# Kernel optimization log

Hardware: AMD Instinct MI355X
Metric: run time of the kernel (lower is better)

## Reference

```python
import jax, jax.numpy as jnp
import numpy as np

B, S, D, H = 2, 2048, 1024, 16
DH = D // H  # 64
NEG = -1000000000.0


def setup_inputs() -> dict:
    key = jax.random.key(0)
    ks = jax.random.split(key, 10)
    scale = 1.0 / np.sqrt(D)
    inp = {
        "x": jax.random.normal(ks[0], (B, S, D), dtype=jnp.float32),
        "mask": jax.random.randint(ks[1], (B, S, S), 0, 2, dtype=jnp.int32),
        "Wq": jax.random.normal(ks[2], (D, D), dtype=jnp.float32) * scale,
        "bq": jnp.zeros((D,), dtype=jnp.float32),
        "Wk": jax.random.normal(ks[3], (D, D), dtype=jnp.float32) * scale,
        "bk": jnp.zeros((D,), dtype=jnp.float32),
        "Wv": jax.random.normal(ks[4], (D, D), dtype=jnp.float32) * scale,
        "bv": jnp.zeros((D,), dtype=jnp.float32),
        "Wo": jax.random.normal(ks[5], (D, D), dtype=jnp.float32) * scale,
        "bo": jnp.zeros((D,), dtype=jnp.float32),
    }
    return inp


def reference(x, mask, Wq, bq, Wk, bk, Wv, bv, Wo, bo):
    b, s, _ = x.shape
    # Linear projections (torch Linear: y = x @ W^T + b), then split heads -> [b,h,s,dh]
    q = (x @ Wq.T + bq).reshape(b, s, H, DH).transpose(0, 2, 1, 3)
    k = (x @ Wk.T + bk).reshape(b, s, H, DH).transpose(0, 2, 1, 3)
    v = (x @ Wv.T + bv).reshape(b, s, H, DH).transpose(0, 2, 1, 3)
    # scores: [b,h,sq,sk]
    scores = jnp.einsum("bhqd,bhkd->bhqk", q, k) / jnp.sqrt(jnp.float32(DH))
    # code masks where mask == 0 (mask broadcast over heads)
    scores = jnp.where(mask[:, None, :, :] == 0, NEG, scores)
    attn = jax.nn.softmax(scores, axis=-1)
    out = jnp.einsum("bhqk,bhkd->bhqd", attn, v)  # [b,h,sq,dh]
    out = out.transpose(0, 2, 1, 3).reshape(b, s, D)  # merge heads -> [b,s,d]
    return out @ Wo.T + bo
```

## Files before the change

### kernel.cpp

```cpp
#include <hip/hip_runtime.h>
#include <stdint.h>

#define SB 2
#define SS 2048
#define SD 1024
#define SH 16
#define SDH 64
#define SM (SB*SS)
#define NEGINF_MASK -1000000000.0f
#define QSCALE 0.18033688011112043f
#define CSHIFT 16.0f

typedef __attribute__((ext_vector_type(8))) short short8;
typedef __attribute__((ext_vector_type(4))) short short4v;
typedef __attribute__((ext_vector_type(4))) float f32x4;
typedef __attribute__((ext_vector_type(4))) float float4v;
typedef __attribute__((ext_vector_type(2))) uint32_t uint2v;

__device__ static inline short f2bf(float f) {
    uint32_t u = __float_as_uint(f);
    u += 0x7fffu + ((u >> 16) & 1u);
    return (short)(u >> 16);
}

__device__ static inline void gload_lds16(const void* g, void* l) {
    __builtin_amdgcn_global_load_lds(
        (__attribute__((address_space(1))) void*)g,
        (__attribute__((address_space(3))) void*)l,
        16, 0, 0);
}

#define NX4 (SM*SD/4)
#define NW4 (SD*SD/4)
__global__ void cvt_all_kernel(const float* __restrict__ x,
                               const float* __restrict__ Wq, const float* __restrict__ Wk,
                               const float* __restrict__ Wv, const float* __restrict__ Wo,
                               short* __restrict__ xb,
                               short* __restrict__ wqb, short* __restrict__ wkb,
                               short* __restrict__ wvb, short* __restrict__ wob) {
    int i = blockIdx.x * 256 + threadIdx.x;
    const float* src; short* dst; int idx;
    if (i < NX4) { src = x; dst = xb; idx = i; }
    else {
        int j = i - NX4;
        int sel = j >> 18;
        idx = j & (NW4 - 1);
        src = (sel == 0) ? Wq : (sel == 1) ? Wk : (sel == 2) ? Wv : Wo;
        dst = (sel == 0) ? wqb : (sel == 1) ? wkb : (sel == 2) ? wvb : wob;
    }
    float4v v = *(const float4v*)(src + (size_t)idx * 4);
    short4v o;
    o[0] = f2bf(v[0]); o[1] = f2bf(v[1]); o[2] = f2bf(v[2]); o[3] = f2bf(v[3]);
    *(short4v*)(dst + (size_t)idx * 4) = o;
}

__global__ void pack_mask_kernel(const int* __restrict__ mask, unsigned long long* __restrict__ bits) {
    unsigned int i = blockIdx.x * 256u + threadIdx.x;
    int pred = mask[i] != 0;
    unsigned long long b = __ballot(pred);
    if ((threadIdx.x & 63u) == 0u) bits[i >> 6] = b;
}

template <typename OutT>
__device__ inline void gemm_bt_body(const short* __restrict__ A, const short* __restrict__ W,
                                    const float* __restrict__ bias, OutT* __restrict__ C,
                                    int M, int N, int K, int rowBase, int colBase, float scale) {
    __shared__ short As[2][128 * 32];
    __shared__ short Bs[2][128 * 32];
    const int tid = threadIdx.x, lane = tid & 63, wid = tid >> 6;
    const int r15 = lane & 15, hi = lane >> 4;
    const int wr = wid >> 1, wc = wid & 1;

    const int chBase0 = wid * 64, chBase1 = 256 + wid * 64;
    const int ch0 = chBase0 + lane, ch1 = chBase1 + lane;
    const short* aP0 = A + (size_t)(rowBase + (ch0 >> 2)) * K + (ch0 & 3) * 8;
    const short* aP1 = A + (size_t)(rowBase + (ch1 >> 2)) * K + (ch1 & 3) * 8;
    const short* bP0 = W + (size_t)(colBase + (ch0 >> 2)) * K + (ch0 & 3) * 8;
    const short* bP1 = W + (size_t)(colBase + (ch1 >> 2)) * K + (ch1 & 3) * 8;

    gload_lds16(aP0, &As[0][chBase0 * 8]);
    gload_lds16(aP1, &As[0][chBase1 * 8]);
    gload_lds16(bP0, &Bs[0][chBase0 * 8]);
    gload_lds16(bP1, &Bs[0][chBase1 * 8]);

    f32x4 acc[4][4] = {};
    const int NIT = K / 32;

    for (int it = 0; it < NIT; ++it) {
        __syncthreads();
        const int cur = it & 1, nxt = cur ^ 1;
        if (it + 1 < NIT) {
            int kt = (it + 1) * 32;
            gload_lds16(aP0 + kt, &As[nxt][chBase0 * 8]);
            gload_lds16(aP1 + kt, &As[nxt][chBase1 * 8]);
            gload_lds16(bP0 + kt, &Bs[nxt][chBase0 * 8]);
            gload_lds16(bP1 + kt, &Bs[nxt][chBase1 * 8]);
        }

        short8 aF[4], bF[4];
#pragma unroll
        for (int mi = 0; mi < 4; ++mi)
            aF[mi] = *(const short8*)&As[cur][(wr * 64 + mi * 16 + r15) * 32 + hi * 8];
#pragma unroll
        for (int ni = 0; ni < 4; ++ni)
            bF[ni] = *(const short8*)&Bs[cur][(wc * 64 + ni * 16 + r15) * 32 + hi * 8];

        __builtin_amdgcn_s_setprio(1);
#pragma unroll
        for (int mi = 0; mi < 4; ++mi)
#pragma unroll
            for (int ni = 0; ni < 4; ++ni)
                acc[mi][ni] = __builtin_amdgcn_mfma_f32_16x16x32_bf16(aF[mi], bF[ni], acc[mi][ni], 0, 0, 0);
        __builtin_amdgcn_s_setprio(0);
    }

#pragma unroll
    for (int ni = 0; ni < 4; ++ni) {
        int col = colBase + wc * 64 + ni * 16 + r15;
        float bv = bias[col];
#pragma unroll
        for (int mi = 0; mi < 4; ++mi) {
#pragma unroll
            for (int r = 0; r < 4; ++r) {
                int row = rowBase + wr * 64 + mi * 16 + hi * 4 + r;
                float v = (acc[mi][ni][r] + bv) * scale;
                if constexpr (sizeof(OutT) == 2) C[(size_t)row * N + col] = f2bf(v);
                else                             C[(size_t)row * N + col] = v;
            }
        }
    }
}

__global__ __launch_bounds__(256, 3) void gemm_qkv_kernel(
    const short* __restrict__ A,
    const short* __restrict__ W0, const short* __restrict__ W1, const short* __restrict__ W2,
    const float* __restrict__ b0, const float* __restrict__ b1, const float* __restrict__ b2,
    short* __restrict__ O0, short* __restrict__ O1, short* __restrict__ O2) {
    const short* W = (blockIdx.z == 0) ? W0 : (blockIdx.z == 1) ? W1 : W2;
    const float* bias = (blockIdx.z == 0) ? b0 : (blockIdx.z == 1) ? b1 : b2;
    short* C = (blockIdx.z == 0) ? O0 : (blockIdx.z == 1) ? O1 : O2;
    float scale = (blockIdx.z == 0) ? QSCALE : 1.0f;
    gemm_bt_body<short>(A, W, bias, C, SM, SD, SD, blockIdx.y * 128, blockIdx.x * 128, scale);
}

__global__ __launch_bounds__(256, 3) void gemm_out_kernel(
    const short* __restrict__ A, const short* __restrict__ W,
    const float* __restrict__ bias, float* __restrict__ C) {
    gemm_bt_body<float>(A, W, bias, C, SM, SD, SD, blockIdx.y * 128, blockIdx.x * 128, 1.0f);
}

__global__ __launch_bounds__(512, 4) void attn_kernel(
    const short* __restrict__ Q, const short* __restrict__ K, const short* __restrict__ V,
    const unsigned long long* __restrict__ mbits, short* __restrict__ O) {
    const int tid = threadIdx.x, lane = tid & 63, wid = tid >> 6;
    const int r15 = lane & 15, hi = lane >> 4;
    const int b = blockIdx.z, h = blockIdx.y;
    const int q0 = blockIdx.x * 128 + wid * 16;
    const int brow = b * SS;

    __shared__ short Ks[2][64 * 64];
    __shared__ short Vt[2][64 * 72];
    __shared__ short Pl[8][16 * 64];
    char* pw = (char*)&Pl[wid][0];

    const short* Kbase = K + (size_t)brow * SD + h * SDH;
    const short* Vbase = V + (size_t)brow * SD + h * SDH;
    const unsigned long long* mrow_p = mbits + (size_t)(brow + q0 + r15) * (SS / 64);

    short8 qF[2];
#pragma unroll
    for (int kd = 0; kd < 2; ++kd)
        qF[kd] = *(const short8*)&Q[(size_t)(brow + q0 + r15) * SD + h * SDH + kd * 32 + hi * 8];

    short8 onesF;
#pragma unroll
    for (int j = 0; j < 8; ++j) onesF[j] = (short)0x3F80;

    f32x4 o[4] = {};
    f32x4 lacc = {};

    const int krow_s = tid >> 3, kcol_s = tid & 7;
    const int vp = tid & 31, vc0 = (tid >> 5) * 4;

    gload_lds16(Kbase + (size_t)krow_s * SD + ((kcol_s ^ (krow_s & 7)) * 8), &Ks[0][wid * 512]);
    short4v va = *(const short4v*)(Vbase + (size_t)(2 * vp) * SD + vc0);
    short4v vb2 = *(const short4v*)(Vbase + (size_t)(2 * vp + 1) * SD + vc0);
    unsigned long long mb = mrow_p[0];
#pragma unroll
    for (int j = 0; j < 4; ++j) {
        uint32_t pk = (uint32_t)(uint16_t)va[j] | ((uint32_t)(uint16_t)vb2[j] << 16);
        *(uint32_t*)&Vt[0][(vc0 + j) * 72 + 2 * vp] = pk;
    }

    for (int t = 0; t < SS / 64; ++t) {
        __syncthreads();
        const int cur = t & 1, nxt = cur ^ 1;
        const int tn = (t < SS / 64 - 1) ? t + 1 : t;

        gload_lds16(Kbase + (size_t)(tn * 64 + krow_s) * SD + ((kcol_s ^ (krow_s & 7)) * 8),
                    &Ks[nxt][wid * 512]);
        va  = *(const short4v*)(Vbase + (size_t)(tn * 64 + 2 * vp) * SD + vc0);
        vb2 = *(const short4v*)(Vbase + (size_t)(tn * 64 + 2 * vp + 1) * SD + vc0);
        unsigned long long mbn = mrow_p[tn];

        f32x4 s[4] = {};
        __builtin_amdgcn_s_setprio(1);
#pragma unroll
        for (int kc = 0; kc < 4; ++kc) {
            int krow = kc * 16 + r15;
#pragma unroll
            for (int kd = 0; kd < 2; ++kd) {
                short8 kF = *(const short8*)&Ks[cur][krow * 64 + (((kd * 4 + hi) ^ (krow & 7)) * 8)];
                s[kc] = __builtin_amdgcn_mfma_f32_16x16x32_bf16(kF, qF[kd], s[kc], 0, 0, 0);
            }
        }
        __builtin_amdgcn_s_setprio(0);

#pragma unroll
        for (int kc = 0; kc < 4; ++kc) {
            unsigned nib = (unsigned)(mb >> (kc * 16 + hi * 4)) & 0xFu;
#pragma unroll
            for (int r = 0; r < 4; ++r) {
                float v = (nib & (1u << r)) ? (s[kc][r] - CSHIFT) : NEGINF_MASK;
                float e;
                asm("v_exp_f32 %0, %1" : "=v"(e) : "v"(v));
                s[kc][r] = e;
            }
        }

#pragma unroll
        for (int kc = 0; kc < 4; ++kc) {
            uint32_t d0, d1;
            asm("v_cvt_pk_bf16_f32 %0, %1, %2" : "=v"(d0) : "v"(s[kc][0]), "v"(s[kc][1]));
            asm("v_cvt_pk_bf16_f32 %0, %1, %2" : "=v"(d1) : "v"(s[kc][2]), "v"(s[kc][3]));
            int chunk = (2 * kc + (hi >> 1)) ^ (r15 & 7);
            uint2v val = { d0, d1 };
            *(uint2v*)(pw + r15 * 128 + chunk * 16 + (hi & 1) * 8) = val;
        }

        short8 pF[2];
#pragma unroll
        for (int kf = 0; kf < 2; ++kf) {
            int chunk = (4 * kf + hi) ^ (r15 & 7);
            pF[kf] = *(const short8*)(pw + r15 * 128 + chunk * 16);
        }

        __builtin_amdgcn_s_setprio(1);
#pragma unroll
        for (int df = 0; df < 4; ++df) {
#pragma unroll
            for (int kf = 0; kf < 2; ++kf) {
                short8 vF = *(const short8*)&Vt[cur][(df * 16 + r15) * 72 + kf * 32 + hi * 8];
                o[df] = __builtin_amdgcn_mfma_f32_16x16x32_bf16(pF[kf], vF, o[df], 0, 0, 0);
            }
        }
        lacc = __builtin_amdgcn_mfma_f32_16x16x32_bf16(pF[0], onesF, lacc, 0, 0, 0);
        lacc = __builtin_amdgcn_mfma_f32_16x16x32_bf16(pF[1], onesF, lacc, 0, 0, 0);
        __builtin_amdgcn_s_setprio(0);

#pragma unroll
        for (int j = 0; j < 4; ++j) {
            uint32_t pk = (uint32_t)(uint16_t)va[j] | ((uint32_t)(uint16_t)vb2[j] << 16);
            *(uint32_t*)&Vt[nxt][(vc0 + j) * 72 + 2 * vp] = pk;
        }
        mb = mbn;
    }

#pragma unroll
    for (int r = 0; r < 4; ++r) {
        float inv = 1.0f / lacc[r];
        size_t row = (size_t)(brow + q0 + hi * 4 + r);
#pragma unroll
        for (int df = 0; df < 4; ++df)
            O[row * SD + h * SDH + df * 16 + r15] = f2bf(o[df][r] * inv);
    }
}

extern "C" void kernel_launch(void* const* d_in, const int* in_sizes, int n_in,
                              void* d_out, int out_size, void* d_ws, size_t ws_size,
                              hipStream_t stream) {
    const float* x  = (const float*)d_in[0];
    const int* mask = (const int*)d_in[1];
    const float* Wq = (const float*)d_in[2];
    const float* bq = (const float*)d_in[3];
    const float* Wk = (const float*)d_in[4];
    const float* bk = (const float*)d_in[5];
    const float* Wv = (const float*)d_in[6];
    const float* bv = (const float*)d_in[7];
    const float* Wo = (const float*)d_in[8];
    const float* bo = (const float*)d_in[9];
    float* out = (float*)d_out;

    char* ws = (char*)d_ws;
    size_t off = 0;
    auto alloc = [&](size_t bytes) { void* p = ws + off; off += (bytes + 255) & ~(size_t)255; return p; };

    short* xb  = (short*)alloc((size_t)SM * SD * 2);
    short* wqb = (short*)alloc((size_t)SD * SD * 2);
    short* wkb = (short*)alloc((size_t)SD * SD * 2);
    short* wvb = (short*)alloc((size_t)SD * SD * 2);
    short* wob = (short*)alloc((size_t)SD * SD * 2);
    short* Qb  = (short*)alloc((size_t)SM * SD * 2);
    short* Kb  = (short*)alloc((size_t)SM * SD * 2);
    short* Vb  = (short*)alloc((size_t)SM * SD * 2);
    short* AOb = (short*)alloc((size_t)SM * SD * 2);
    unsigned long long* mbits = (unsigned long long*)alloc((size_t)SB * SS * (SS / 64) * 8);

    cvt_all_kernel<<<(NX4 + 4 * NW4) / 256, 256, 0, stream>>>(
        x, Wq, Wk, Wv, Wo, xb, wqb, wkb, wvb, wob);
    pack_mask_kernel<<<SB * SS * SS / 256, 256, 0, stream>>>(mask, mbits);

    gemm_qkv_kernel<<<dim3(SD / 128, SM / 128, 3), 256, 0, stream>>>(
        xb, wqb, wkb, wvb, bq, bk, bv, Qb, Kb, Vb);

    attn_kernel<<<dim3(SS / 128, SH, SB), 512, 0, stream>>>(Qb, Kb, Vb, mbits, AOb);

    gemm_out_kernel<<<dim3(SD / 128, SM / 128), 256, 0, stream>>>(AOb, wob, bo, out);
}
```

Measured before the change: 148.7 us.

## Split attention waves into 2x4 query/key-half grid with LDS partial-sum reduction

```diff
diff --git a/kernel.cpp b/kernel.cpp
--- a/kernel.cpp
+++ b/kernel.cpp
@@ -155,7 +155,8 @@
     const int tid = threadIdx.x, lane = tid & 63, wid = tid >> 6;
     const int r15 = lane & 15, hi = lane >> 4;
     const int b = blockIdx.z, h = blockIdx.y;
-    const int q0 = blockIdx.x * 128 + wid * 16;
+    const int qc = wid & 3, kh = wid >> 2;
+    const int q0 = blockIdx.x * 128 + qc * 32;
     const int brow = b * SS;
 
     __shared__ short Ks[2][64 * 64];
@@ -165,19 +166,22 @@
 
     const short* Kbase = K + (size_t)brow * SD + h * SDH;
     const short* Vbase = V + (size_t)brow * SD + h * SDH;
-    const unsigned long long* mrow_p = mbits + (size_t)(brow + q0 + r15) * (SS / 64);
-
-    short8 qF[2];
-#pragma unroll
-    for (int kd = 0; kd < 2; ++kd)
-        qF[kd] = *(const short8*)&Q[(size_t)(brow + q0 + r15) * SD + h * SDH + kd * 32 + hi * 8];
+    const unsigned long long* mp0 = mbits + (size_t)(brow + q0 + r15) * (SS / 64);
+    const unsigned long long* mp1 = mbits + (size_t)(brow + q0 + 16 + r15) * (SS / 64);
+
+    short8 qF[2][2];
+#pragma unroll
+    for (int c = 0; c < 2; ++c)
+#pragma unroll
+        for (int kd = 0; kd < 2; ++kd)
+            qF[c][kd] = *(const short8*)&Q[(size_t)(brow + q0 + c * 16 + r15) * SD + h * SDH + kd * 32 + hi * 8];
 
     short8 onesF;
 #pragma unroll
     for (int j = 0; j < 8; ++j) onesF[j] = (short)0x3F80;
 
-    f32x4 o[4] = {};
-    f32x4 lacc = {};
+    f32x4 o[2][4] = {};
+    f32x4 lacc[2] = {};
 
     const int krow_s = tid >> 3, kcol_s = tid & 7;
     const int vp = tid & 31, vc0 = (tid >> 5) * 4;
@@ -185,7 +189,7 @@
     gload_lds16(Kbase + (size_t)krow_s * SD + ((kcol_s ^ (krow_s & 7)) * 8), &Ks[0][wid * 512]);
     short4v va = *(const short4v*)(Vbase + (size_t)(2 * vp) * SD + vc0);
     short4v vb2 = *(const short4v*)(Vbase + (size_t)(2 * vp + 1) * SD + vc0);
-    unsigned long long mb = mrow_p[0];
+    unsigned long long mb[2] = { mp0[0], mp1[0] };
 #pragma unroll
     for (int j = 0; j < 4; ++j) {
         uint32_t pk = (uint32_t)(uint16_t)va[j] | ((uint32_t)(uint16_t)vb2[j] << 16);
@@ -201,61 +205,57 @@
                     &Ks[nxt][wid * 512]);
         va  = *(const short4v*)(Vbase + (size_t)(tn * 64 + 2 * vp) * SD + vc0);
         vb2 = *(const short4v*)(Vbase + (size_t)(tn * 64 + 2 * vp + 1) * SD + vc0);
-        unsigned long long mbn = mrow_p[tn];
-
-        f32x4 s[4] = {};
+        unsigned long long mbn0 = mp0[tn], mbn1 = mp1[tn];
+
+        f32x4 s[2][2] = {};
         __builtin_amdgcn_s_setprio(1);
 #pragma unroll
-        for (int kc = 0; kc < 4; ++kc) {
-            int krow = kc * 16 + r15;
+        for (int kc = 0; kc < 2; ++kc) {
+            int krow = kh * 32 + kc * 16 + r15;
 #pragma unroll
             for (int kd = 0; kd < 2; ++kd) {
                 short8 kF = *(const short8*)&Ks[cur][krow * 64 + (((kd * 4 + hi) ^ (krow & 7)) * 8)];
-                s[kc] = __builtin_amdgcn_mfma_f32_16x16x32_bf16(kF, qF[kd], s[kc], 0, 0, 0);
+                s[0][kc] = __builtin_amdgcn_mfma_f32_16x16x32_bf16(kF, qF[0][kd], s[0][kc], 0, 0, 0);
+                s[1][kc] = __builtin_amdgcn_mfma_f32_16x16x32_bf16(kF, qF[1][kd], s[1][kc], 0, 0, 0);
             }
         }
         __builtin_amdgcn_s_setprio(0);
 
-#pragma unroll
-        for (int kc = 0; kc < 4; ++kc) {
-            unsigned nib = (unsigned)(mb >> (kc * 16 + hi * 4)) & 0xFu;
-#pragma unroll
-            for (int r = 0; r < 4; ++r) {
-                float v = (nib & (1u << r)) ? (s[kc][r] - CSHIFT) : NEGINF_MASK;
-                float e;
-                asm("v_exp_f32 %0, %1" : "=v"(e) : "v"(v));
-                s[kc][r] = e;
+        short8 pF[2];
+#pragma unroll
+        for (int c = 0; c < 2; ++c) {
+            unsigned long long mbc = (c == 0) ? mb[0] : mb[1];
+            char* pc = pw + c * 1024;
+#pragma unroll
+            for (int kc = 0; kc < 2; ++kc) {
+                unsigned nib = (unsigned)(mbc >> (kh * 32 + kc * 16 + hi * 4)) & 0xFu;
+#pragma unroll
+                for (int r = 0; r < 4; ++r) {
+                    float v = (nib & (1u << r)) ? (s[c][kc][r] - CSHIFT) : NEGINF_MASK;
+                    float e;
+                    asm("v_exp_f32 %0, %1" : "=v"(e) : "v"(v));
+                    s[c][kc][r] = e;
+                }
+                uint32_t d0, d1;
+                asm("v_cvt_pk_bf16_f32 %0, %1, %2" : "=v"(d0) : "v"(s[c][kc][0]), "v"(s[c][kc][1]));
+                asm("v_cvt_pk_bf16_f32 %0, %1, %2" : "=v"(d1) : "v"(s[c][kc][2]), "v"(s[c][kc][3]));
+                int chunk = (2 * kc + (hi >> 1)) ^ (r15 & 3);
+                uint2v val = { d0, d1 };
+                *(uint2v*)(pc + r15 * 64 + chunk * 16 + (hi & 1) * 8) = val;
             }
-        }
-
-#pragma unroll
-        for (int kc = 0; kc < 4; ++kc) {
-            uint32_t d0, d1;
-            asm("v_cvt_pk_bf16_f32 %0, %1, %2" : "=v"(d0) : "v"(s[kc][0]), "v"(s[kc][1]));
-            asm("v_cvt_pk_bf16_f32 %0, %1, %2" : "=v"(d1) : "v"(s[kc][2]), "v"(s[kc][3]));
-            int chunk = (2 * kc + (hi >> 1)) ^ (r15 & 7);
-            uint2v val = { d0, d1 };
-            *(uint2v*)(pw + r15 * 128 + chunk * 16 + (hi & 1) * 8) = val;
-        }
-
-        short8 pF[2];
-#pragma unroll
-        for (int kf = 0; kf < 2; ++kf) {
-            int chunk = (4 * kf + hi) ^ (r15 & 7);
-            pF[kf] = *(const short8*)(pw + r15 * 128 + chunk * 16);
+            int rchunk = hi ^ (r15 & 3);
+            pF[c] = *(const short8*)(pc + r15 * 64 + rchunk * 16);
         }
 
         __builtin_amdgcn_s_setprio(1);
 #pragma unroll
         for (int df = 0; df < 4; ++df) {
-#pragma unroll
-            for (int kf = 0; kf < 2; ++kf) {
-                short8 vF = *(const short8*)&Vt[cur][(df * 16 + r15) * 72 + kf * 32 + hi * 8];
-                o[df] = __builtin_amdgcn_mfma_f32_16x16x32_bf16(pF[kf], vF, o[df], 0, 0, 0);
-            }
-        }
-        lacc = __builtin_amdgcn_mfma_f32_16x16x32_bf16(pF[0], onesF, lacc, 0, 0, 0);
-        lacc = __builtin_amdgcn_mfma_f32_16x16x32_bf16(pF[1], onesF, lacc, 0, 0, 0);
+            short8 vF = *(const short8*)&Vt[cur][(df * 16 + r15) * 72 + kh * 32 + hi * 8];
+            o[0][df] = __builtin_amdgcn_mfma_f32_16x16x32_bf16(pF[0], vF, o[0][df], 0, 0, 0);
+            o[1][df] = __builtin_amdgcn_mfma_f32_16x16x32_bf16(pF[1], vF, o[1][df], 0, 0, 0);
+        }
+        lacc[0] = __builtin_amdgcn_mfma_f32_16x16x32_bf16(pF[0], onesF, lacc[0], 0, 0, 0);
+        lacc[1] = __builtin_amdgcn_mfma_f32_16x16x32_bf16(pF[1], onesF, lacc[1], 0, 0, 0);
         __builtin_amdgcn_s_setprio(0);
 
 #pragma unroll
@@ -263,17 +263,59 @@
             uint32_t pk = (uint32_t)(uint16_t)va[j] | ((uint32_t)(uint16_t)vb2[j] << 16);
             *(uint32_t*)&Vt[nxt][(vc0 + j) * 72 + 2 * vp] = pk;
         }
-        mb = mbn;
-    }
-
-#pragma unroll
-    for (int r = 0; r < 4; ++r) {
-        float inv = 1.0f / lacc[r];
-        size_t row = (size_t)(brow + q0 + hi * 4 + r);
-#pragma unroll
-        for (int df = 0; df < 4; ++df)
-            O[row * SD + h * SDH + df * 16 + r15] = f2bf(o[df][r] * inv);
-    }
+        mb[0] = mbn0; mb[1] = mbn1;
+    }
+
+    float* lbase = (float*)&Ks[0][0];
+    float* obase = (float*)&Pl[0][0];
+
+#define PUBLISH(slot)                                                            \
+    {                                                                            \
+        float* mbf = obase + (slot) * 2048;                                      \
+        _Pragma("unroll")                                                        \
+        for (int c = 0; c < 2; ++c)                                              \
+            _Pragma("unroll")                                                    \
+            for (int df = 0; df < 4; ++df)                                       \
+                _Pragma("unroll")                                                \
+                for (int r = 0; r < 4; ++r)                                      \
+                    mbf[(c * 16 + hi * 4 + r) * 64 + df * 16 + r15] = o[c][df][r]; \
+        if (r15 == 0) {                                                          \
+            _Pragma("unroll")                                                    \
+            for (int c = 0; c < 2; ++c)                                          \
+                _Pragma("unroll")                                                \
+                for (int r = 0; r < 4; ++r)                                      \
+                    lbase[(slot) * 32 + c * 16 + hi * 4 + r] = lacc[c][r];       \
+        }                                                                        \
+    }
+
+#define CONSUME(slot)                                                            \
+    {                                                                            \
+        float* mbf = obase + (slot) * 2048;                                      \
+        _Pragma("unroll")                                                        \
+        for (int c = 0; c < 2; ++c)                                              \
+            _Pragma("unroll")                                                    \
+            for (int r = 0; r < 4; ++r) {                                        \
+                float lt = lacc[c][r] + lbase[(slot) * 32 + c * 16 + hi * 4 + r];\
+                float inv = 1.0f / lt;                                           \
+                size_t row = (size_t)(brow + q0 + c * 16 + hi * 4 + r);          \
+                _Pragma("unroll")                                                \
+                for (int df = 0; df < 4; ++df) {                                 \
+                    float ot = o[c][df][r] + mbf[(c * 16 + hi * 4 + r) * 64 + df * 16 + r15]; \
+                    O[row * SD + h * SDH + df * 16 + r15] = f2bf(ot * inv);      \
+                }                                                                \
+            }                                                                    \
+    }
+
+    __syncthreads();
+    if (kh == 1 && qc < 2) PUBLISH(qc);
+    __syncthreads();
+    if (kh == 0 && qc < 2) CONSUME(qc);
+    __syncthreads();
+    if (kh == 1 && qc >= 2) PUBLISH(qc - 2);
+    __syncthreads();
+    if (kh == 0 && qc >= 2) CONSUME(qc - 2);
+#undef PUBLISH
+#undef CONSUME
 }
 
 extern "C" void kernel_launch(void* const* d_in, const int* in_sizes, int n_in,
```

Result: slower. 154.4 us (+3.9%).

## Keep softmax probabilities in registers via permuted V layout; retile output GEMM

Applied to the files above, without the earlier changes.

```diff
diff --git a/kernel.cpp b/kernel.cpp
--- a/kernel.cpp
+++ b/kernel.cpp
@@ -15,7 +15,7 @@
 typedef __attribute__((ext_vector_type(4))) short short4v;
 typedef __attribute__((ext_vector_type(4))) float f32x4;
 typedef __attribute__((ext_vector_type(4))) float float4v;
-typedef __attribute__((ext_vector_type(2))) uint32_t uint2v;
+typedef __attribute__((ext_vector_type(4))) uint32_t uint4v;
 
 __device__ static inline short f2bf(float f) {
     uint32_t u = __float_as_uint(f);
@@ -61,10 +61,18 @@
     if ((threadIdx.x & 63u) == 0u) bits[i >> 6] = b;
 }
 
-template <typename OutT>
-__device__ inline void gemm_bt_body(const short* __restrict__ A, const short* __restrict__ W,
-                                    const float* __restrict__ bias, OutT* __restrict__ C,
-                                    int M, int N, int K, int rowBase, int colBase, float scale) {
+__global__ __launch_bounds__(256, 3) void gemm_qkv_kernel(
+    const short* __restrict__ A,
+    const short* __restrict__ W0, const short* __restrict__ W1, const short* __restrict__ W2,
+    const float* __restrict__ b0, const float* __restrict__ b1, const float* __restrict__ b2,
+    short* __restrict__ O0, short* __restrict__ O1, short* __restrict__ O2) {
+    const short* W = (blockIdx.z == 0) ? W0 : (blockIdx.z == 1) ? W1 : W2;
+    const float* bias = (blockIdx.z == 0) ? b0 : (blockIdx.z == 1) ? b1 : b2;
+    short* C = (blockIdx.z == 0) ? O0 : (blockIdx.z == 1) ? O1 : O2;
+    const float scale = (blockIdx.z == 0) ? QSCALE : 1.0f;
+    const int rowBase = blockIdx.y * 128, colBase = blockIdx.x * 128;
+    const int K = SD, N = SD;
+
     __shared__ short As[2][128 * 32];
     __shared__ short Bs[2][128 * 32];
     const int tid = threadIdx.x, lane = tid & 63, wid = tid >> 6;
@@ -123,30 +131,76 @@
 #pragma unroll
             for (int r = 0; r < 4; ++r) {
                 int row = rowBase + wr * 64 + mi * 16 + hi * 4 + r;
-                float v = (acc[mi][ni][r] + bv) * scale;
-                if constexpr (sizeof(OutT) == 2) C[(size_t)row * N + col] = f2bf(v);
-                else                             C[(size_t)row * N + col] = v;
-            }
-        }
-    }
-}
-
-__global__ __launch_bounds__(256, 3) void gemm_qkv_kernel(
-    const short* __restrict__ A,
-    const short* __restrict__ W0, const short* __restrict__ W1, const short* __restrict__ W2,
-    const float* __restrict__ b0, const float* __restrict__ b1, const float* __restrict__ b2,
-    short* __restrict__ O0, short* __restrict__ O1, short* __restrict__ O2) {
-    const short* W = (blockIdx.z == 0) ? W0 : (blockIdx.z == 1) ? W1 : W2;
-    const float* bias = (blockIdx.z == 0) ? b0 : (blockIdx.z == 1) ? b1 : b2;
-    short* C = (blockIdx.z == 0) ? O0 : (blockIdx.z == 1) ? O1 : O2;
-    float scale = (blockIdx.z == 0) ? QSCALE : 1.0f;
-    gemm_bt_body<short>(A, W, bias, C, SM, SD, SD, blockIdx.y * 128, blockIdx.x * 128, scale);
-}
-
-__global__ __launch_bounds__(256, 3) void gemm_out_kernel(
+                C[(size_t)row * N + col] = f2bf((acc[mi][ni][r] + bv) * scale);
+            }
+        }
+    }
+}
+
+__global__ __launch_bounds__(256, 2) void gemm_out_kernel(
     const short* __restrict__ A, const short* __restrict__ W,
     const float* __restrict__ bias, float* __restrict__ C) {
-    gemm_bt_body<float>(A, W, bias, C, SM, SD, SD, blockIdx.y * 128, blockIdx.x * 128, 1.0f);
+    const int rowBase = blockIdx.y * 128, colBase = blockIdx.x * 64;
+    const int K = SD, N = SD;
+
+    __shared__ short As[2][128 * 32];
+    __shared__ short Bs[2][64 * 32];
+    const int tid = threadIdx.x, lane = tid & 63, wid = tid >> 6;
+    const int r15 = lane & 15, hi = lane >> 4;
+
+    const int chBase0 = wid * 64, chBase1 = 256 + wid * 64;
+    const int ch0 = chBase0 + lane, ch1 = chBase1 + lane;
+    const short* aP0 = A + (size_t)(rowBase + (ch0 >> 2)) * K + (ch0 & 3) * 8;
+    const short* aP1 = A + (size_t)(rowBase + (ch1 >> 2)) * K + (ch1 & 3) * 8;
+    const short* bP0 = W + (size_t)(colBase + (ch0 >> 2)) * K + (ch0 & 3) * 8;
+
+    gload_lds16(aP0, &As[0][chBase0 * 8]);
+    gload_lds16(aP1, &As[0][chBase1 * 8]);
+    gload_lds16(bP0, &Bs[0][chBase0 * 8]);
+
+    f32x4 acc[2][4] = {};
+    const int NIT = K / 32;
+
+    for (int it = 0; it < NIT; ++it) {
+        __syncthreads();
+        const int cur = it & 1, nxt = cur ^ 1;
+        if (it + 1 < NIT) {
+            int kt = (it + 1) * 32;
+            gload_lds16(aP0 + kt, &As[nxt][chBase0 * 8]);
+            gload_lds16(aP1 + kt, &As[nxt][chBase1 * 8]);
+            gload_lds16(bP0 + kt, &Bs[nxt][chBase0 * 8]);
+        }
+
+        short8 aF[2], bF[4];
+#pragma unroll
+        for (int mi = 0; mi < 2; ++mi)
+            aF[mi] = *(const short8*)&As[cur][(wid * 32 + mi * 16 + r15) * 32 + hi * 8];
+#pragma unroll
+        for (int ni = 0; ni < 4; ++ni)
+            bF[ni] = *(const short8*)&Bs[cur][(ni * 16 + r15) * 32 + hi * 8];
+
+        __builtin_amdgcn_s_setprio(1);
+#pragma unroll
+        for (int mi = 0; mi < 2; ++mi)
+#pragma unroll
+            for (int ni = 0; ni < 4; ++ni)
+                acc[mi][ni] = __builtin_amdgcn_mfma_f32_16x16x32_bf16(aF[mi], bF[ni], acc[mi][ni], 0, 0, 0);
+        __builtin_amdgcn_s_setprio(0);
+    }
+
+#pragma unroll
+    for (int ni = 0; ni < 4; ++ni) {
+        int col = colBase + ni * 16 + r15;
+        float bv = bias[col];
+#pragma unroll
+        for (int mi = 0; mi < 2; ++mi) {
+#pragma unroll
+            for (int r = 0; r < 4; ++r) {
+                int row = rowBase + wid * 32 + mi * 16 + hi * 4 + r;
+                C[(size_t)row * N + col] = acc[mi][ni][r] + bv;
+            }
+        }
+    }
 }
 
 __global__ __launch_bounds__(512, 4) void attn_kernel(
@@ -160,8 +214,6 @@
 
     __shared__ short Ks[2][64 * 64];
     __shared__ short Vt[2][64 * 72];
-    __shared__ short Pl[8][16 * 64];
-    char* pw = (char*)&Pl[wid][0];
 
     const short* Kbase = K + (size_t)brow * SD + h * SDH;
     const short* Vbase = V + (size_t)brow * SD + h * SDH;
@@ -181,15 +233,17 @@
 
     const int krow_s = tid >> 3, kcol_s = tid & 7;
     const int vp = tid & 31, vc0 = (tid >> 5) * 4;
+    const int k2 = 2 * vp;
+    const int vcol = (k2 & 32) | ((k2 & 12) << 1) | ((k2 & 16) >> 2) | (k2 & 3);
 
     gload_lds16(Kbase + (size_t)krow_s * SD + ((kcol_s ^ (krow_s & 7)) * 8), &Ks[0][wid * 512]);
-    short4v va = *(const short4v*)(Vbase + (size_t)(2 * vp) * SD + vc0);
-    short4v vb2 = *(const short4v*)(Vbase + (size_t)(2 * vp + 1) * SD + vc0);
+    short4v va = *(const short4v*)(Vbase + (size_t)k2 * SD + vc0);
+    short4v vb2 = *(const short4v*)(Vbase + (size_t)(k2 + 1) * SD + vc0);
     unsigned long long mb = mrow_p[0];
 #pragma unroll
     for (int j = 0; j < 4; ++j) {
         uint32_t pk = (uint32_t)(uint16_t)va[j] | ((uint32_t)(uint16_t)vb2[j] << 16);
-        *(uint32_t*)&Vt[0][(vc0 + j) * 72 + 2 * vp] = pk;
+        *(uint32_t*)&Vt[0][(vc0 + j) * 72 + vcol] = pk;
     }
 
     for (int t = 0; t < SS / 64; ++t) {
@@ -199,8 +253,8 @@
 
         gload_lds16(Kbase + (size_t)(tn * 64 + krow_s) * SD + ((kcol_s ^ (krow_s & 7)) * 8),
                     &Ks[nxt][wid * 512]);
-        va  = *(const short4v*)(Vbase + (size_t)(tn * 64 + 2 * vp) * SD + vc0);
-        vb2 = *(const short4v*)(Vbase + (size_t)(tn * 64 + 2 * vp + 1) * SD + vc0);
+        va  = *(const short4v*)(Vbase + (size_t)(tn * 64 + k2) * SD + vc0);
+        vb2 = *(const short4v*)(Vbase + (size_t)(tn * 64 + k2 + 1) * SD + vc0);
         unsigned long long mbn = mrow_p[tn];
 
         f32x4 s[4] = {};
@@ -228,21 +282,16 @@
             }
         }
 
-#pragma unroll
-        for (int kc = 0; kc < 4; ++kc) {
-            uint32_t d0, d1;
-            asm("v_cvt_pk_bf16_f32 %0, %1, %2" : "=v"(d0) : "v"(s[kc][0]), "v"(s[kc][1]));
-            asm("v_cvt_pk_bf16_f32 %0, %1, %2" : "=v"(d1) : "v"(s[kc][2]), "v"(s[kc][3]));
-            int chunk = (2 * kc + (hi >> 1)) ^ (r15 & 7);
-            uint2v val = { d0, d1 };
-            *(uint2v*)(pw + r15 * 128 + chunk * 16 + (hi & 1) * 8) = val;
-        }
-
         short8 pF[2];
 #pragma unroll
         for (int kf = 0; kf < 2; ++kf) {
-            int chunk = (4 * kf + hi) ^ (r15 & 7);
-            pF[kf] = *(const short8*)(pw + r15 * 128 + chunk * 16);
+            uint32_t w0, w1, w2, w3;
+            asm("v_cvt_pk_bf16_f32 %0, %1, %2" : "=v"(w0) : "v"(s[2 * kf][0]),     "v"(s[2 * kf][1]));
+            asm("v_cvt_pk_bf16_f32 %0, %1, %2" : "=v"(w1) : "v"(s[2 * kf][2]),     "v"(s[2 * kf][3]));
+            asm("v_cvt_pk_bf16_f32 %0, %1, %2" : "=v"(w2) : "v"(s[2 * kf + 1][0]), "v"(s[2 * kf + 1][1]));
+            asm("v_cvt_pk_bf16_f32 %0, %1, %2" : "=v"(w3) : "v"(s[2 * kf + 1][2]), "v"(s[2 * kf + 1][3]));
+            uint4v t4 = { w0, w1, w2, w3 };
+            pF[kf] = __builtin_bit_cast(short8, t4);
         }
 
         __builtin_amdgcn_s_setprio(1);
@@ -261,7 +310,7 @@
 #pragma unroll
         for (int j = 0; j < 4; ++j) {
             uint32_t pk = (uint32_t)(uint16_t)va[j] | ((uint32_t)(uint16_t)vb2[j] << 16);
-            *(uint32_t*)&Vt[nxt][(vc0 + j) * 72 + 2 * vp] = pk;
+            *(uint32_t*)&Vt[nxt][(vc0 + j) * 72 + vcol] = pk;
         }
         mb = mbn;
     }
@@ -315,5 +364,5 @@
 
     attn_kernel<<<dim3(SS / 128, SH, SB), 512, 0, stream>>>(Qb, Kb, Vb, mbits, AOb);
 
-    gemm_out_kernel<<<dim3(SD / 128, SM / 128), 256, 0, stream>>>(AOb, wob, bo, out);
-}
+    gemm_out_kernel<<<dim3(SD / 64, SM / 128), 256, 0, stream>>>(AOb, wob, bo, out);
+}
```

Result: faster. 142.8 us (-3.9%).
